# Kernel tuning notes

Measured on AMD Instinct MI355X. Metric: run time of the kernel, lower is better.

## Reference

```python
import jax, jax.numpy as jnp
import numpy as np

N = 262144        # tokens routed
D = 1024          # input_dim
E = 64            # num_experts
TOP_K = 2
NOISE_EPS = 1e-05
ALPHA = 10.0


def setup_inputs() -> dict:
    key = jax.random.key(0)
    k1, k2, k3, k4, k5 = jax.random.split(key, 5)
    x = jax.random.normal(k1, (N, D), dtype=jnp.float32)
    # nn.Linear init scale ~ 1/sqrt(fan_in); keep logits at sane magnitude
    gate_w = jax.random.normal(k2, (E, D), dtype=jnp.float32) * (1.0 / np.sqrt(D))
    gate_b = jax.random.normal(k3, (E,), dtype=jnp.float32) * 0.01
    # w_noise is initialized to zeros in the module; use small random values
    # so the noise path is exercised
    w_noise = jax.random.normal(k4, (E, E), dtype=jnp.float32) * 0.01
    noise = jax.random.normal(k5, (N, E), dtype=jnp.float32)  # torch.randn_like
    return {"x": x, "gate_w": gate_w, "gate_b": gate_b,
            "w_noise": w_noise, "noise": noise}


def reference(x, gate_w, gate_b, w_noise, noise):
    # gate linear: [N, D] @ [D, E] + [E]
    clean_logits = jnp.einsum('nd,ed->ne', x, gate_w) + gate_b
    # training-mode learnable noise injection
    raw_noise_stddev = clean_logits @ w_noise                 # [N, E]
    noise_stddev = jax.nn.softplus(raw_noise_stddev) + NOISE_EPS
    logits = clean_logits + noise * noise_stddev              # noisy_logits

    # decompostion_tp: k-th largest per row (kthvalue(n - k + 1) == k-th largest)
    kth_largest = jax.lax.top_k(logits, TOP_K)[0][:, -1]       # [N]
    mask = logits < kth_largest[:, None]                       # strictly below kth
    sm = jax.nn.softmax(logits, axis=1)
    out = jnp.where(mask,
                    ALPHA * jnp.log1p(sm),      # alpha * log(sm + 1)
                    ALPHA * jnp.expm1(sm))      # alpha * (exp(sm) - 1)

    gates = jax.nn.softmax(out, axis=1)
    return gates
```

## Files before the change

### kernel.cpp

```cpp
#include <hip/hip_runtime.h>

typedef _Float16 half8v __attribute__((ext_vector_type(8)));
typedef float f32x4 __attribute__((ext_vector_type(4)));

constexpr float INV4096 = 1.0f / 4096.0f;
constexpr float ALPHA = 10.0f;

__device__ __forceinline__ f32x4 mfma16(half8v a, half8v b, f32x4 c_) {
  return __builtin_amdgcn_mfma_f32_16x16x32_f16(a, b, c_, 0, 0, 0);
}
__device__ __forceinline__ void dma16(const void *g, void *l) {
  __builtin_amdgcn_global_load_lds(
      (const __attribute__((address_space(1))) void *)g,
      (__attribute__((address_space(3))) void *)l, 16, 0, 0);
}
template <int N> __device__ __forceinline__ void wait_vm() {
  asm volatile("s_waitcnt vmcnt(%0)" ::"n"(N) : "memory");
}

__global__ __launch_bounds__(256) void presplit(const float *__restrict__ GW,
                                                const float *__restrict__ WN,
                                                char *__restrict__ ws) {
  const int b = blockIdx.x;
  const int tid = threadIdx.x;
  if (b < 64) {
    int idx = b * 256 + tid;
    int e = idx >> 8;
    int c4 = idx & 255;
    f32x4 v = *reinterpret_cast<const f32x4 *>(GW + (size_t)idx * 4);
#pragma unroll
    for (int j = 0; j < 4; ++j) {
      int k = c4 * 4 + j;
      float vv = v[j];
      _Float16 hh = (_Float16)vv;
      _Float16 ll = (_Float16)((vv - (float)hh) * 4096.0f);
      int ck = k >> 6, kk = k & 63;
      int off = ck * 16384 + e * 128 + ((((kk >> 3) ^ (e & 7))) << 4) + ((kk & 7) << 1);
      *reinterpret_cast<_Float16 *>(ws + off) = hh;
      *reinterpret_cast<_Float16 *>(ws + off + 8192) = ll;
    }
  } else {
    int idx = (b - 64) * 256 + tid;
    int k = idx >> 4;
    int e0 = (idx & 15) << 2;
    f32x4 v = *reinterpret_cast<const f32x4 *>(WN + (size_t)k * 64 + e0);
#pragma unroll
    for (int j = 0; j < 4; ++j) {
      int e = e0 + j;
      float vv = v[j];
      _Float16 hh = (_Float16)vv;
      _Float16 ll = (_Float16)((vv - (float)hh) * 4096.0f);
      int off = 262144 + e * 128 + ((((k >> 3) ^ (e & 7))) << 4) + ((k & 7) << 1);
      *reinterpret_cast<_Float16 *>(ws + off) = hh;
      *reinterpret_cast<_Float16 *>(ws + off + 8192) = ll;
    }
  }
}

__global__ __launch_bounds__(256, 2) void topk_gating(
    const float *__restrict__ X, const char *__restrict__ WS,
    const float *__restrict__ GB, const float *__restrict__ NZ,
    float *__restrict__ OUT) {
  __shared__ __align__(16) char lds[65536];
  const int tid = threadIdx.x;
  const int lane = tid & 63;
  const int wv = tid >> 6;
  const int q = lane >> 4;
  const int c = lane & 15;
  const int waveRow = blockIdx.x * 64 + wv * 16;

  f32x4 accH[4] = {};
  f32x4 accX[4] = {};
  f32x4 aR[4][4];

  const float *xBase = X + (size_t)(waveRow + c) * 1024 + q * 8;
  const char *wsL = WS + wv * 1024 + lane * 16;
  char *ldsL = lds + wv * 1024;

#define CONV(A, ah, al)                                           \
  {                                                               \
    _Pragma("unroll") for (int ks_ = 0; ks_ < 2; ++ks_)           \
        _Pragma("unroll") for (int j_ = 0; j_ < 8; ++j_) {        \
      float xv_ = A[ks_ * 2 + (j_ >> 2)][j_ & 3];                 \
      _Float16 hh_ = (_Float16)xv_;                               \
      ah[ks_][j_] = hh_;                                          \
      al[ks_][j_] = (_Float16)((xv_ - (float)hh_) * 4096.0f);     \
    }                                                             \
  }
#define MFMAB(BUF, ah, al)                                                 \
  {                                                                        \
    _Pragma("unroll") for (int ks_ = 0; ks_ < 2; ++ks_)                    \
        _Pragma("unroll") for (int t_ = 0; t_ < 4; ++t_) {                 \
      int e_ = t_ * 16 + c;                                                \
      int off_ = (BUF) + e_ * 128 + ((((ks_ * 4 + q) ^ (e_ & 7))) << 4);   \
      half8v bh_ = *reinterpret_cast<half8v *>(lds + off_);                \
      half8v bl_ = *reinterpret_cast<half8v *>(lds + off_ + 8192);         \
      accH[t_] = mfma16(ah[ks_], bh_, accH[t_]);                           \
      accX[t_] = mfma16(ah[ks_], bl_, accX[t_]);                           \
      accX[t_] = mfma16(al[ks_], bh_, accX[t_]);                           \
    }                                                                      \
  }
#define BAR() __builtin_amdgcn_s_barrier()

#pragma unroll
  for (int m = 0; m < 4; ++m) {
#pragma unroll
    for (int j = 0; j < 4; ++j)
#pragma unroll
      for (int i = 0; i < 4; ++i)
        dma16(wsL + (m * 4 + j) * 16384 + i * 4096,
              ldsL + j * 16384 + i * 4096);
#pragma unroll
    for (int s = 0; s < 4; ++s) {
      const float *xp = xBase + (m * 4 + s) * 64;
      aR[s][0] = *(const f32x4 *)(xp + 0);
      aR[s][1] = *(const f32x4 *)(xp + 4);
      aR[s][2] = *(const f32x4 *)(xp + 32);
      aR[s][3] = *(const f32x4 *)(xp + 36);
    }
    wait_vm<0>();
    BAR();
#pragma unroll
    for (int s = 0; s < 4; ++s) {
      half8v ah[2], al[2];
      CONV(aR[s], ah, al);
      MFMAB(s * 16384, ah, al);
    }
    BAR();
  }

  float bs0 = GB[c], bs1 = GB[16 + c], bs2 = GB[32 + c], bs3 = GB[48 + c];
#pragma unroll
  for (int i = 0; i < 4; ++i)
    dma16(wsL + 262144 + i * 4096, ldsL + i * 4096);
  asm volatile("" ::: "memory");
  float nz[4][4];
#pragma unroll
  for (int t = 0; t < 4; ++t)
#pragma unroll
    for (int r = 0; r < 4; ++r)
      nz[t][r] = NZ[(size_t)(waveRow + 4 * q + r) * 64 + t * 16 + c];

  float cl[4][4];
  const float bsv[4] = {bs0, bs1, bs2, bs3};
#pragma unroll
  for (int t = 0; t < 4; ++t)
#pragma unroll
    for (int r = 0; r < 4; ++r)
      cl[t][r] = accH[t][r] + accX[t][r] * INV4096 + bsv[t];

  char *cb = lds + 16384 + wv * 4096;
#pragma unroll
  for (int t = 0; t < 4; ++t)
#pragma unroll
    for (int r = 0; r < 4; ++r) {
      int row = 4 * q + r;
      int colf = t * 16 + c;
      int off = row * 256 + ((((colf >> 2) ^ row)) << 4) + ((colf & 3) << 2);
      *reinterpret_cast<float *>(cb + off) = cl[t][r];
    }
  wait_vm<16>();
  BAR();

  f32x4 rH[4] = {};
  f32x4 rX[4] = {};
#pragma unroll
  for (int ks = 0; ks < 2; ++ks) {
    int slot0 = ks * 8 + q * 2;
    f32x4 va = *reinterpret_cast<f32x4 *>(cb + c * 256 + (((slot0 ^ c)) << 4));
    f32x4 vb = *reinterpret_cast<f32x4 *>(cb + c * 256 + ((((slot0 + 1) ^ c)) << 4));
    half8v ah, al;
#pragma unroll
    for (int j = 0; j < 4; ++j) {
      float v = va[j];
      _Float16 hh = (_Float16)v;
      ah[j] = hh;
      al[j] = (_Float16)((v - (float)hh) * 4096.0f);
      float v2 = vb[j];
      _Float16 h2 = (_Float16)v2;
      ah[4 + j] = h2;
      al[4 + j] = (_Float16)((v2 - (float)h2) * 4096.0f);
    }
#pragma unroll
    for (int t = 0; t < 4; ++t) {
      int e = t * 16 + c;
      int off = e * 128 + ((((ks * 4 + q) ^ (e & 7))) << 4);
      half8v bh = *reinterpret_cast<half8v *>(lds + off);
      half8v bl = *reinterpret_cast<half8v *>(lds + off + 8192);
      rH[t] = mfma16(ah, bh, rH[t]);
      rX[t] = mfma16(ah, bl, rX[t]);
      rX[t] = mfma16(al, bh, rX[t]);
    }
  }

  float lg[4][4];
#pragma unroll
  for (int t = 0; t < 4; ++t)
#pragma unroll
    for (int r = 0; r < 4; ++r) {
      float raw = rH[t][r] + rX[t][r] * INV4096;
      float sp = fmaxf(raw, 0.0f) + __logf(1.0f + __expf(-fabsf(raw)));
      lg[r][t] = cl[t][r] + nz[t][r] * (sp + 1e-5f);
    }

#pragma unroll
  for (int r = 0; r < 4; ++r) {
    float v0 = lg[r][0], v1 = lg[r][1], v2 = lg[r][2], v3 = lg[r][3];
    float a = fmaxf(v0, v1), b_ = fminf(v0, v1);
    float d1 = fmaxf(v2, v3), d2 = fminf(v2, v3);
    float m1 = fmaxf(a, d1);
    float m2 = fmaxf(fminf(a, d1), fmaxf(b_, d2));
#pragma unroll
    for (int s = 1; s <= 8; s <<= 1) {
      float om1 = __shfl_xor(m1, s, 64);
      float om2 = __shfl_xor(m2, s, 64);
      float hi = fmaxf(m1, om1);
      float lo = fminf(m1, om1);
      float sec = (m1 >= om1) ? m2 : om2;
      m2 = fmaxf(lo, sec);
      m1 = hi;
    }
    float se[4], ssum = 0.f;
#pragma unroll
    for (int t = 0; t < 4; ++t) {
      se[t] = __expf(lg[r][t] - m1);
      ssum += se[t];
    }
#pragma unroll
    for (int s = 1; s <= 8; s <<= 1) ssum += __shfl_xor(ssum, s, 64);
    float inv = 1.0f / ssum;
    float ov[4];
#pragma unroll
    for (int t = 0; t < 4; ++t) {
      float sm = se[t] * inv;
      float vlog = ALPHA * __logf(1.0f + sm);
      float vexp = ALPHA * (__expf(sm) - 1.0f);
      ov[t] = (lg[r][t] < m2) ? vlog : vexp;
    }
    float g = fmaxf(fmaxf(ov[0], ov[1]), fmaxf(ov[2], ov[3]));
#pragma unroll
    for (int s = 1; s <= 8; s <<= 1) g = fmaxf(g, __shfl_xor(g, s, 64));
    float gsum = 0.f;
#pragma unroll
    for (int t = 0; t < 4; ++t) {
      ov[t] = __expf(ov[t] - g);
      gsum += ov[t];
    }
#pragma unroll
    for (int s = 1; s <= 8; s <<= 1) gsum += __shfl_xor(gsum, s, 64);
    float ginv = 1.0f / gsum;
    size_t rowOff = (size_t)(waveRow + 4 * q + r) * 64;
#pragma unroll
    for (int t = 0; t < 4; ++t)
      OUT[rowOff + t * 16 + c] = ov[t] * ginv;
  }
}

extern "C" void kernel_launch(void *const *d_in, const int *in_sizes, int n_in,
                              void *d_out, int out_size, void *d_ws,
                              size_t ws_size, hipStream_t stream) {
  const float *x = (const float *)d_in[0];
  const float *gw = (const float *)d_in[1];
  const float *gb = (const float *)d_in[2];
  const float *wn = (const float *)d_in[3];
  const float *nz = (const float *)d_in[4];
  float *out = (float *)d_out;
  char *ws = (char *)d_ws;
  const int N = in_sizes[0] / 1024;

  hipLaunchKernelGGL(presplit, dim3(68), dim3(256), 0, stream, gw, wn, ws);
  hipLaunchKernelGGL(topk_gating, dim3(N / 64), dim3(256), 0, stream, x, ws,
                     gb, nz, out);
}
```

Measured before the change: 296.6 us.

## Software-pipeline gate GEMM with staged X through LDS and triple-buffered weights

Replaces the four-phase load-then-compute loop with a sixteen-step software pipeline. X rows are loaded coalesced into registers two steps ahead and written to a swizzled, double-buffered LDS tile. Weight chunks are DMA'd into a triple-buffered LDS ring, so global loads overlap MFMA work instead of stalling at full vmcnt waits. LDS grows from 64KB to 80KB, which may limit blocks per CU, and there are more barriers per K-chunk.

```diff
diff --git a/kernel.cpp b/kernel.cpp
--- a/kernel.cpp
+++ b/kernel.cpp
@@ -17,6 +17,12 @@
 template <int N> __device__ __forceinline__ void wait_vm() {
   asm volatile("s_waitcnt vmcnt(%0)" ::"n"(N) : "memory");
 }
+#define FENCE() asm volatile("" ::: "memory")
+#define BAR()                            \
+  do {                                   \
+    __builtin_amdgcn_s_barrier();        \
+    __builtin_amdgcn_sched_barrier(0);   \
+  } while (0)
 
 __global__ __launch_bounds__(256) void presplit(const float *__restrict__ GW,
                                                 const float *__restrict__ WN,
@@ -61,79 +67,118 @@
     const float *__restrict__ X, const char *__restrict__ WS,
     const float *__restrict__ GB, const float *__restrict__ NZ,
     float *__restrict__ OUT) {
-  __shared__ __align__(16) char lds[65536];
+  __shared__ __align__(16) char lds[81920];
   const int tid = threadIdx.x;
   const int lane = tid & 63;
   const int wv = tid >> 6;
   const int q = lane >> 4;
   const int c = lane & 15;
-  const int waveRow = blockIdx.x * 64 + wv * 16;
+  const int blockRow = blockIdx.x * 64;
+  const int waveRow = blockRow + wv * 16;
+
+  const int r0 = lane >> 3, s0 = lane & 7;
+  const float *pC0 = X + (size_t)(waveRow + r0) * 1024 + s0 * 4;
+  const float *pC1 = pC0 + 32;
+  const float *pC2 = pC0 + 8 * 1024;
+  const float *pC3 = pC2 + 32;
+  const int aswz = wv * 4096 + r0 * 256 + ((s0 ^ r0) << 4);
+  const char *wsL = WS + wv * 1024 + lane * 16;
+  const int aRdB = wv * 4096 + (c << 8);
+  const int xr = (c & 7) << 4;
 
   f32x4 accH[4] = {};
   f32x4 accX[4] = {};
-  f32x4 aR[4][4];
-
-  const float *xBase = X + (size_t)(waveRow + c) * 1024 + q * 8;
-  const char *wsL = WS + wv * 1024 + lane * 16;
-  char *ldsL = lds + wv * 1024;
-
-#define CONV(A, ah, al)                                           \
-  {                                                               \
-    _Pragma("unroll") for (int ks_ = 0; ks_ < 2; ++ks_)           \
-        _Pragma("unroll") for (int j_ = 0; j_ < 8; ++j_) {        \
-      float xv_ = A[ks_ * 2 + (j_ >> 2)][j_ & 3];                 \
-      _Float16 hh_ = (_Float16)xv_;                               \
-      ah[ks_][j_] = hh_;                                          \
-      al[ks_][j_] = (_Float16)((xv_ - (float)hh_) * 4096.0f);     \
-    }                                                             \
-  }
-#define MFMAB(BUF, ah, al)                                                 \
-  {                                                                        \
-    _Pragma("unroll") for (int ks_ = 0; ks_ < 2; ++ks_)                    \
-        _Pragma("unroll") for (int t_ = 0; t_ < 4; ++t_) {                 \
-      int e_ = t_ * 16 + c;                                                \
-      int off_ = (BUF) + e_ * 128 + ((((ks_ * 4 + q) ^ (e_ & 7))) << 4);   \
-      half8v bh_ = *reinterpret_cast<half8v *>(lds + off_);                \
-      half8v bl_ = *reinterpret_cast<half8v *>(lds + off_ + 8192);         \
-      accH[t_] = mfma16(ah[ks_], bh_, accH[t_]);                           \
-      accX[t_] = mfma16(ah[ks_], bl_, accX[t_]);                           \
-      accX[t_] = mfma16(al[ks_], bh_, accX[t_]);                           \
-    }                                                                      \
-  }
-#define BAR() __builtin_amdgcn_s_barrier()
-
-#pragma unroll
-  for (int m = 0; m < 4; ++m) {
-#pragma unroll
-    for (int j = 0; j < 4; ++j)
-#pragma unroll
-      for (int i = 0; i < 4; ++i)
-        dma16(wsL + (m * 4 + j) * 16384 + i * 4096,
-              ldsL + j * 16384 + i * 4096);
-#pragma unroll
-    for (int s = 0; s < 4; ++s) {
-      const float *xp = xBase + (m * 4 + s) * 64;
-      aR[s][0] = *(const f32x4 *)(xp + 0);
-      aR[s][1] = *(const f32x4 *)(xp + 4);
-      aR[s][2] = *(const f32x4 *)(xp + 32);
-      aR[s][3] = *(const f32x4 *)(xp + 36);
-    }
-    wait_vm<0>();
-    BAR();
-#pragma unroll
-    for (int s = 0; s < 4; ++s) {
-      half8v ah[2], al[2];
-      CONV(aR[s], ah, al);
-      MFMAB(s * 16384, ah, al);
-    }
-    BAR();
-  }
+  f32x4 rA[4];
+
+#define ALOAD(KC)                                   \
+  {                                                 \
+    rA[0] = *(const f32x4 *)(pC0 + (KC) * 64);      \
+    rA[1] = *(const f32x4 *)(pC1 + (KC) * 64);      \
+    rA[2] = *(const f32x4 *)(pC2 + (KC) * 64);      \
+    rA[3] = *(const f32x4 *)(pC3 + (KC) * 64);      \
+  }
+#define DSWA(KC)                                          \
+  {                                                       \
+    char *aw_ = lds + ((KC) % 2) * 16384 + aswz;          \
+    *reinterpret_cast<f32x4 *>(aw_) = rA[0];              \
+    *reinterpret_cast<f32x4 *>(aw_ + 128) = rA[1];        \
+    *reinterpret_cast<f32x4 *>(aw_ + 2048) = rA[2];       \
+    *reinterpret_cast<f32x4 *>(aw_ + 2176) = rA[3];       \
+  }
+#define BDMA(KC)                                                      \
+  {                                                                   \
+    char *bd_ = lds + 32768 + ((KC) % 3) * 16384 + wv * 1024;         \
+    _Pragma("unroll") for (int i_ = 0; i_ < 4; ++i_)                  \
+        dma16(wsL + (KC) * 16384 + i_ * 4096, bd_ + i_ * 4096);       \
+  }
+#define STEPC(KC)                                                            \
+  {                                                                          \
+    const int ab_ = ((KC) % 2) * 16384;                                      \
+    const int bb_ = 32768 + ((KC) % 3) * 16384;                              \
+    _Pragma("unroll") for (int ks_ = 0; ks_ < 2; ++ks_) {                    \
+      int s0_ = ((ks_ * 8 + q * 2) << 4) ^ xr;                               \
+      f32x4 va_ = *reinterpret_cast<f32x4 *>(lds + ab_ + aRdB + s0_);        \
+      f32x4 vb_ = *reinterpret_cast<f32x4 *>(lds + ab_ + aRdB + (s0_ ^ 16)); \
+      half8v ah_, al_;                                                       \
+      _Pragma("unroll") for (int j_ = 0; j_ < 4; ++j_) {                     \
+        float v1_ = va_[j_], v2_ = vb_[j_];                                  \
+        _Float16 h1_ = (_Float16)v1_, h2_ = (_Float16)v2_;                   \
+        ah_[j_] = h1_;                                                       \
+        al_[j_] = (_Float16)((v1_ - (float)h1_) * 4096.0f);                  \
+        ah_[4 + j_] = h2_;                                                   \
+        al_[4 + j_] = (_Float16)((v2_ - (float)h2_) * 4096.0f);              \
+      }                                                                      \
+      _Pragma("unroll") for (int t_ = 0; t_ < 4; ++t_) {                     \
+        int e_ = t_ * 16 + c;                                                \
+        int off_ = bb_ + e_ * 128 + ((((ks_ * 4 + q) ^ (e_ & 7))) << 4);     \
+        half8v bh_ = *reinterpret_cast<half8v *>(lds + off_);                \
+        half8v bl_ = *reinterpret_cast<half8v *>(lds + off_ + 8192);         \
+        accH[t_] = mfma16(ah_, bh_, accH[t_]);                               \
+        accX[t_] = mfma16(ah_, bl_, accX[t_]);                               \
+        accX[t_] = mfma16(al_, bh_, accX[t_]);                               \
+      }                                                                      \
+    }                                                                        \
+  }
+#define STEP(N)                          \
+  {                                      \
+    if ((N) + 1 <= 15) DSWA((N) + 1);    \
+    FENCE();                             \
+    if ((N) + 2 <= 15) ALOAD((N) + 2);   \
+    FENCE();                             \
+    if ((N) + 2 <= 15) BDMA((N) + 2);    \
+    FENCE();                             \
+    STEPC(N);                            \
+  }
+
+  ALOAD(0); FENCE();
+  DSWA(0);  FENCE();
+  ALOAD(1); FENCE();
+  BDMA(0);  FENCE();
+  BDMA(1);  FENCE();
+  wait_vm<4>(); BAR();
+
+  STEP(0)  wait_vm<8>(); BAR();
+  STEP(1)  wait_vm<8>(); BAR();
+  STEP(2)  wait_vm<8>(); BAR();
+  STEP(3)  wait_vm<8>(); BAR();
+  STEP(4)  wait_vm<8>(); BAR();
+  STEP(5)  wait_vm<8>(); BAR();
+  STEP(6)  wait_vm<8>(); BAR();
+  STEP(7)  wait_vm<8>(); BAR();
+  STEP(8)  wait_vm<8>(); BAR();
+  STEP(9)  wait_vm<8>(); BAR();
+  STEP(10) wait_vm<8>(); BAR();
+  STEP(11) wait_vm<8>(); BAR();
+  STEP(12) wait_vm<8>(); BAR();
+  STEP(13) wait_vm<8>(); BAR();
+  STEP(14) wait_vm<0>(); BAR();
+  STEP(15)
 
   float bs0 = GB[c], bs1 = GB[16 + c], bs2 = GB[32 + c], bs3 = GB[48 + c];
 #pragma unroll
   for (int i = 0; i < 4; ++i)
-    dma16(wsL + 262144 + i * 4096, ldsL + i * 4096);
-  asm volatile("" ::: "memory");
+    dma16(wsL + 262144 + i * 4096, lds + 49152 + wv * 1024 + i * 4096);
+  FENCE();
   float nz[4][4];
 #pragma unroll
   for (int t = 0; t < 4; ++t)
@@ -149,7 +194,7 @@
     for (int r = 0; r < 4; ++r)
       cl[t][r] = accH[t][r] + accX[t][r] * INV4096 + bsv[t];
 
-  char *cb = lds + 16384 + wv * 4096;
+  char *cb = lds + 65536 + wv * 4096;
 #pragma unroll
   for (int t = 0; t < 4; ++t)
 #pragma unroll
@@ -184,7 +229,7 @@
 #pragma unroll
     for (int t = 0; t < 4; ++t) {
       int e = t * 16 + c;
-      int off = e * 128 + ((((ks * 4 + q) ^ (e & 7))) << 4);
+      int off = 49152 + e * 128 + ((((ks * 4 + q) ^ (e & 7))) << 4);
       half8v bh = *reinterpret_cast<half8v *>(lds + off);
       half8v bl = *reinterpret_cast<half8v *>(lds + off + 8192);
       rH[t] = mfma16(ah, bh, rH[t]);
```

Measured after the change: 280.3 us. -5.5%, faster.

## Software-pipeline weight DMA and X loads with triple-buffered LDS, 512-thread blocks

Applied to the files above, without the earlier changes.

Replaces the four-stage load-all-then-compute loop with a 16-step software pipeline. Gate-weight chunks are DMA'd two steps ahead into a 3-slot LDS ring, and X fragments are double-buffered in registers one step ahead. Blocks grow to 512 threads (128 rows) with 48KB LDS and a launch bound of 4, so the weight staging is shared by more rows. This is meant to hide global load latency behind MFMA work and raise residency, at the cost of a barrier every step and more register pressure from the tighter launch bound.

```diff
diff --git a/kernel.cpp b/kernel.cpp
--- a/kernel.cpp
+++ b/kernel.cpp
@@ -17,6 +17,12 @@
 template <int N> __device__ __forceinline__ void wait_vm() {
   asm volatile("s_waitcnt vmcnt(%0)" ::"n"(N) : "memory");
 }
+#define FENCE() asm volatile("" ::: "memory")
+#define BAR()                            \
+  do {                                   \
+    __builtin_amdgcn_s_barrier();        \
+    __builtin_amdgcn_sched_barrier(0);   \
+  } while (0)
 
 __global__ __launch_bounds__(256) void presplit(const float *__restrict__ GW,
                                                 const float *__restrict__ WN,
@@ -57,26 +63,38 @@
   }
 }
 
-__global__ __launch_bounds__(256, 2) void topk_gating(
+__global__ __launch_bounds__(512, 4) void topk_gating(
     const float *__restrict__ X, const char *__restrict__ WS,
     const float *__restrict__ GB, const float *__restrict__ NZ,
     float *__restrict__ OUT) {
-  __shared__ __align__(16) char lds[65536];
+  __shared__ __align__(16) char lds[49152];
   const int tid = threadIdx.x;
   const int lane = tid & 63;
   const int wv = tid >> 6;
   const int q = lane >> 4;
   const int c = lane & 15;
-  const int waveRow = blockIdx.x * 64 + wv * 16;
+  const int waveRow = blockIdx.x * 128 + wv * 16;
 
   f32x4 accH[4] = {};
   f32x4 accX[4] = {};
-  f32x4 aR[4][4];
+  f32x4 a0[4], a1[4];
 
   const float *xBase = X + (size_t)(waveRow + c) * 1024 + q * 8;
-  const char *wsL = WS + wv * 1024 + lane * 16;
-  char *ldsL = lds + wv * 1024;
-
+  const char *wsL = WS + wv * 2048 + lane * 16;
+
+#define LDA4(dst, p)                        \
+  {                                         \
+    dst[0] = *(const f32x4 *)((p) + 0);     \
+    dst[1] = *(const f32x4 *)((p) + 4);     \
+    dst[2] = *(const f32x4 *)((p) + 32);    \
+    dst[3] = *(const f32x4 *)((p) + 36);    \
+  }
+#define BDMA(CK)                                                      \
+  {                                                                   \
+    char *bd_ = lds + ((CK) % 3) * 16384 + wv * 2048;                 \
+    dma16(wsL + (CK) * 16384, bd_);                                   \
+    dma16(wsL + (CK) * 16384 + 1024, bd_ + 1024);                     \
+  }
 #define CONV(A, ah, al)                                           \
   {                                                               \
     _Pragma("unroll") for (int ks_ = 0; ks_ < 2; ++ks_)           \
@@ -100,40 +118,44 @@
       accX[t_] = mfma16(al[ks_], bh_, accX[t_]);                           \
     }                                                                      \
   }
-#define BAR() __builtin_amdgcn_s_barrier()
-
-#pragma unroll
-  for (int m = 0; m < 4; ++m) {
-#pragma unroll
-    for (int j = 0; j < 4; ++j)
-#pragma unroll
-      for (int i = 0; i < 4; ++i)
-        dma16(wsL + (m * 4 + j) * 16384 + i * 4096,
-              ldsL + j * 16384 + i * 4096);
-#pragma unroll
-    for (int s = 0; s < 4; ++s) {
-      const float *xp = xBase + (m * 4 + s) * 64;
-      aR[s][0] = *(const f32x4 *)(xp + 0);
-      aR[s][1] = *(const f32x4 *)(xp + 4);
-      aR[s][2] = *(const f32x4 *)(xp + 32);
-      aR[s][3] = *(const f32x4 *)(xp + 36);
-    }
-    wait_vm<0>();
-    BAR();
-#pragma unroll
-    for (int s = 0; s < 4; ++s) {
-      half8v ah[2], al[2];
-      CONV(aR[s], ah, al);
-      MFMAB(s * 16384, ah, al);
-    }
-    BAR();
-  }
+#define STEP(N, AC, AN)                                          \
+  {                                                              \
+    half8v ah[2], al[2];                                         \
+    if ((N) + 1 <= 15) LDA4(AN, xBase + ((N) + 1) * 64);         \
+    FENCE();                                                     \
+    if ((N) + 2 <= 15) BDMA((N) + 2);                            \
+    FENCE();                                                     \
+    CONV(AC, ah, al);                                            \
+    MFMAB(((N) % 3) * 16384, ah, al);                            \
+  }
+
+  BDMA(0); FENCE();
+  LDA4(a0, xBase); FENCE();
+  BDMA(1); FENCE();
+  wait_vm<6>(); BAR();
+
+  STEP(0, a0, a1)  wait_vm<6>(); BAR();
+  STEP(1, a1, a0)  wait_vm<6>(); BAR();
+  STEP(2, a0, a1)  wait_vm<6>(); BAR();
+  STEP(3, a1, a0)  wait_vm<6>(); BAR();
+  STEP(4, a0, a1)  wait_vm<6>(); BAR();
+  STEP(5, a1, a0)  wait_vm<6>(); BAR();
+  STEP(6, a0, a1)  wait_vm<6>(); BAR();
+  STEP(7, a1, a0)  wait_vm<6>(); BAR();
+  STEP(8, a0, a1)  wait_vm<6>(); BAR();
+  STEP(9, a1, a0)  wait_vm<6>(); BAR();
+  STEP(10, a0, a1) wait_vm<6>(); BAR();
+  STEP(11, a1, a0) wait_vm<6>(); BAR();
+  STEP(12, a0, a1) wait_vm<6>(); BAR();
+  STEP(13, a1, a0) wait_vm<6>(); BAR();
+  STEP(14, a0, a1) wait_vm<4>(); BAR();
+  STEP(15, a1, a0)
+  BAR();
 
   float bs0 = GB[c], bs1 = GB[16 + c], bs2 = GB[32 + c], bs3 = GB[48 + c];
-#pragma unroll
-  for (int i = 0; i < 4; ++i)
-    dma16(wsL + 262144 + i * 4096, ldsL + i * 4096);
-  asm volatile("" ::: "memory");
+  dma16(wsL + 262144, lds + 32768 + wv * 2048);
+  dma16(wsL + 262144 + 1024, lds + 32768 + wv * 2048 + 1024);
+  FENCE();
   float nz[4][4];
 #pragma unroll
   for (int t = 0; t < 4; ++t)
@@ -149,7 +171,7 @@
     for (int r = 0; r < 4; ++r)
       cl[t][r] = accH[t][r] + accX[t][r] * INV4096 + bsv[t];
 
-  char *cb = lds + 16384 + wv * 4096;
+  char *cb = lds + wv * 4096;
 #pragma unroll
   for (int t = 0; t < 4; ++t)
 #pragma unroll
@@ -184,7 +206,7 @@
 #pragma unroll
     for (int t = 0; t < 4; ++t) {
       int e = t * 16 + c;
-      int off = e * 128 + ((((ks * 4 + q) ^ (e & 7))) << 4);
+      int off = 32768 + e * 128 + ((((ks * 4 + q) ^ (e & 7))) << 4);
       half8v bh = *reinterpret_cast<half8v *>(lds + off);
       half8v bl = *reinterpret_cast<half8v *>(lds + off + 8192);
       rH[t] = mfma16(ah, bh, rH[t]);
@@ -269,6 +291,6 @@
   const int N = in_sizes[0] / 1024;
 
   hipLaunchKernelGGL(presplit, dim3(68), dim3(256), 0, stream, gw, wn, ws);
-  hipLaunchKernelGGL(topk_gating, dim3(N / 64), dim3(256), 0, stream, x, ws,
+  hipLaunchKernelGGL(topk_gating, dim3(N / 128), dim3(512), 0, stream, x, ws,
                      gb, nz, out);
 }
```

New measurement: 270.5 us. 1.1x faster.
